# Kernel optimization log

Measured on AMD Instinct MI355X. Metric: run time of the kernel, lower is better.

The kernel has to match this reference:

```python
import jax, jax.numpy as jnp
import numpy as np

NUM_HEADS = 8
OUT_FEATS = 64
TOPK_T = 10          # settings['T']
NEG_INF = -9e15

N_NODES = 8192
IN_FEATS = 512
N_EDGES = 262144  # avg degree 32


def setup_inputs() -> dict:
    key = jax.random.key(0)
    k1, k2, k3, k4, k5 = jax.random.split(key, 5)
    feat = jax.random.normal(k1, (N_NODES, IN_FEATS), jnp.float32)
    # xavier-ish scale for the fc weight [H*D, in_feats]
    fc_weight = jax.random.normal(k2, (NUM_HEADS * OUT_FEATS, IN_FEATS), jnp.float32) * 0.05
    trans_m = jax.random.uniform(k3, (N_EDGES,), jnp.float32)
    src = jax.random.randint(k4, (N_EDGES,), 0, N_NODES, dtype=jnp.int32)
    dst = jax.random.randint(k5, (N_EDGES,), 0, N_NODES, dtype=jnp.int32)
    return {"feat": feat, "fc_weight": fc_weight, "trans_m": trans_m, "src": src, "dst": dst}


def reference(feat, fc_weight, trans_m, src, dst):
    N = feat.shape[0]
    # fc projection -> [N, H, D]
    feat_src = (feat @ fc_weight.T).reshape(N, NUM_HEADS, OUT_FEATS)
    # per-edge per-head dot-product score (SDDMM; same math as the gathered NxN matmul)
    fs, fd = feat_src[src], feat_src[dst]           # [Ne, H, D]
    e = jnp.einsum('ehd,ehd->eh', fs, fd)           # [Ne, H]
    # sparse attn values = sum over heads of e * trans_m, scattered into dense [N, N]
    vals = (e * trans_m[:, None]).sum(-1)           # [Ne]
    attn_dense = jnp.zeros((N, N), feat.dtype).at[src, dst].add(vals)
    # topk mask per row: threshold = clamp(kth largest, min=0); below -> -9e15
    thresh = jnp.maximum(jax.lax.top_k(attn_dense, TOPK_T)[0][:, -1], 0.0)  # [N]
    masked = jnp.where(attn_dense < thresh[:, None], NEG_INF, attn_dense)
    # attn = masked.T ; gather attn[src, dst] == masked[dst, src]; mask edges where < -100
    cond = masked[dst, src] < -100.0                # [Ne]
    e = jnp.where(cond[:, None], NEG_INF, e)
    # edge_softmax over incoming edges of each dst node
    emax = jax.ops.segment_max(e, dst, num_segments=N)        # [N, H]
    e_exp = jnp.exp(e - emax[dst])                            # [Ne, H]
    esum = jax.ops.segment_sum(e_exp, dst, num_segments=N)    # [N, H]
    a = e_exp / esum[dst]                                     # [Ne, H]
    # u_mul_e + sum aggregation: rst[v] = sum_{(u,v) in E} a * feat_src[u]
    rst = jax.ops.segment_sum(a[:, :, None] * fs, dst, num_segments=N)  # [N, H, D]
    return rst
```

## Files before the change

kernel.cpp:

```cpp
#include <hip/hip_runtime.h>
#include <hip/hip_bf16.h>
#include <math.h>

#define N_NODES 8192
#define IN_FEATS 512
#define N_EDGES 262144
#define NUM_HEADS 8
#define OUT_FEATS 64
#define HD (NUM_HEADS * OUT_FEATS)
#define TOPK 10
#define NEG_INF -9e15f
#define MAXD 128
#define EID_MASK 0x3FFFF

__device__ __forceinline__ int swz(int row, int k4) {
  return k4 ^ (4 * (((row & 7) ^ ((row >> 3) & 7)) & 7));
}

__global__ __launch_bounds__(512, 2) void gemm_nt(const float* __restrict__ A,
                                                  const float* __restrict__ B,
                                                  float* __restrict__ C,
                                                  ushort* __restrict__ C16) {
  __shared__ char smem[65536];
  int tid = threadIdx.x;
  int sub = tid >> 8;
  int stid = tid & 255;
  int tx = stid & 15, ty = stid >> 4;
  int brow = blockIdx.x * 128, bcol = blockIdx.y * 128;
  int kbase = sub * 256;

  float (*Asub)[32] = (float(*)[32])(smem + sub * 16384);
  float (*Bsub)[32] = (float(*)[32])(smem + 32768 + sub * 16384);

  int sr = stid >> 1;
  int skc = (stid & 1) * 8;
  const float* gA = A + (size_t)(brow + sr) * IN_FEATS + kbase + skc;
  const float* gB = B + (size_t)(bcol + sr) * IN_FEATS + kbase + skc;
  int w0 = swz(sr, skc), w1 = swz(sr, skc + 4);

  float acc[8][8];
#pragma unroll
  for (int i = 0; i < 8; i++)
#pragma unroll
    for (int j = 0; j < 8; j++) acc[i][j] = 0.f;

  float4 ra0 = *(const float4*)gA;
  float4 ra1 = *(const float4*)(gA + 4);
  float4 rb0 = *(const float4*)gB;
  float4 rb1 = *(const float4*)(gB + 4);

  const int NT = 16;
  for (int t = 0; t < NT; ++t) {
    __syncthreads();
    *(float4*)&Asub[sr][w0] = ra0; *(float4*)&Asub[sr][w1] = ra1;
    *(float4*)&Bsub[sr][w0] = rb0; *(float4*)&Bsub[sr][w1] = rb1;
    if (t + 1 < NT) {
      const float* pA = gA + (t + 1) * 16;
      const float* pB = gB + (t + 1) * 16;
      ra0 = *(const float4*)pA; ra1 = *(const float4*)(pA + 4);
      rb0 = *(const float4*)pB; rb1 = *(const float4*)(pB + 4);
    }
    __syncthreads();
#pragma unroll
    for (int g = 0; g < 4; ++g) {
      float4 av[8], bv[8];
#pragma unroll
      for (int i = 0; i < 8; i++) {
        int r = ty * 8 + i;
        av[i] = *(const float4*)&Asub[r][swz(r, g * 4)];
      }
#pragma unroll
      for (int j = 0; j < 8; j++) {
        int c = tx * 8 + j;
        bv[j] = *(const float4*)&Bsub[c][swz(c, g * 4)];
      }
#pragma unroll
      for (int i = 0; i < 8; i++)
#pragma unroll
        for (int j = 0; j < 8; j++) {
          acc[i][j] = fmaf(av[i].x, bv[j].x, acc[i][j]);
          acc[i][j] = fmaf(av[i].y, bv[j].y, acc[i][j]);
          acc[i][j] = fmaf(av[i].z, bv[j].z, acc[i][j]);
          acc[i][j] = fmaf(av[i].w, bv[j].w, acc[i][j]);
        }
    }
  }

  float (*xch)[33] = (float(*)[33])smem;
  __syncthreads();
#pragma unroll
  for (int r = 0; r < 2; ++r) {
    if (sub == 1) {
#pragma unroll
      for (int k = 0; k < 32; ++k) {
        int idx = r * 32 + k;
        xch[stid][k] = acc[idx >> 3][idx & 7];
      }
    }
    __syncthreads();
    if (sub == 0) {
#pragma unroll
      for (int k = 0; k < 32; ++k) {
        int idx = r * 32 + k;
        acc[idx >> 3][idx & 7] += xch[stid][k];
      }
    }
    __syncthreads();
  }

  if (sub == 0) {
#pragma unroll
    for (int i = 0; i < 8; i++) {
      int row = brow + ty * 8 + i;
      float* cp = C + (size_t)row * HD + bcol + tx * 8;
      *(float4*)cp = make_float4(acc[i][0], acc[i][1], acc[i][2], acc[i][3]);
      *(float4*)(cp + 4) = make_float4(acc[i][4], acc[i][5], acc[i][6], acc[i][7]);
      ushort u[8];
#pragma unroll
      for (int j = 0; j < 8; j++) u[j] = __bfloat16_as_ushort(__float2bfloat16(acc[i][j]));
      uint4 q;
      q.x = (unsigned)u[0] | ((unsigned)u[1] << 16);
      q.y = (unsigned)u[2] | ((unsigned)u[3] << 16);
      q.z = (unsigned)u[4] | ((unsigned)u[5] << 16);
      q.w = (unsigned)u[6] | ((unsigned)u[7] << 16);
      *(uint4*)(C16 + (size_t)row * HD + bcol + tx * 8) = q;
    }
  }
}

__global__ __launch_bounds__(256) void histo(const int* __restrict__ src, const int* __restrict__ dst,
                                             int* __restrict__ cnt_s, int* __restrict__ cnt_d) {
  int e = blockIdx.x * blockDim.x + threadIdx.x;
  if (e < N_EDGES) {
    atomicAdd(&cnt_s[src[e]], 1);
    atomicAdd(&cnt_d[dst[e]], 1);
  }
}

__global__ __launch_bounds__(1024) void scan2(const int* __restrict__ cnt_s, const int* __restrict__ cnt_d,
                                              int* __restrict__ rp_s, int* __restrict__ rp_d) {
  __shared__ int ls[1024];
  const int* cnt = blockIdx.x ? cnt_d : cnt_s;
  int* rp = blockIdx.x ? rp_d : rp_s;
  int t = threadIdx.x;
  int base = t * 8;
  int v[8]; int s = 0;
#pragma unroll
  for (int i = 0; i < 8; i++) { v[i] = cnt[base + i]; s += v[i]; }
  ls[t] = s;
  __syncthreads();
  for (int off = 1; off < 1024; off <<= 1) {
    int x = (t >= off) ? ls[t - off] : 0;
    __syncthreads();
    ls[t] += x;
    __syncthreads();
  }
  int excl = (t == 0) ? 0 : ls[t - 1];
#pragma unroll
  for (int i = 0; i < 8; i++) { rp[base + i] = excl; excl += v[i]; }
  if (t == 1023) rp[N_NODES] = excl;
}

__global__ __launch_bounds__(256) void scatter_csr(const int* __restrict__ src, const int* __restrict__ dst,
                                                   const int* __restrict__ rp_s, const int* __restrict__ rp_d,
                                                   int* __restrict__ fill_s, int* __restrict__ fill_d,
                                                   int* __restrict__ cs, int* __restrict__ cd) {
  int e = blockIdx.x * blockDim.x + threadIdx.x;
  if (e < N_EDGES) {
    int p = rp_s[src[e]] + atomicAdd(&fill_s[src[e]], 1);
    cs[p] = e;
    int q = rp_d[dst[e]] + atomicAdd(&fill_d[dst[e]], 1);
    cd[q] = e;
  }
}

__global__ __launch_bounds__(256) void sort_rows_bitonic(const int* __restrict__ rp_s,
                                                         const int* __restrict__ rp_d,
                                                         const int* __restrict__ dst,
                                                         int* __restrict__ cs, int* __restrict__ cd,
                                                         int* __restrict__ keys_s) {
  int wave = (blockIdx.x * blockDim.x + threadIdx.x) >> 6;
  int lane = threadIdx.x & 63;
  bool is_s = wave < N_NODES;
  int r = is_s ? wave : wave - N_NODES;
  const int* rp = is_s ? rp_s : rp_d;
  int b = rp[r], e2 = rp[r + 1];
  int len = e2 - b; if (len > 128) len = 128;

  int x0 = 0x7FFFFFFF, x1 = 0x7FFFFFFF;
  if (lane < len) {
    int e = is_s ? cs[b + lane] : cd[b + lane];
    x0 = is_s ? ((dst[e] << 18) | e) : e;
  }
  if (lane + 64 < len) {
    int e = is_s ? cs[b + lane + 64] : cd[b + lane + 64];
    x1 = is_s ? ((dst[e] << 18) | e) : e;
  }

  for (int s = 2; s <= 64; s <<= 1) {
    bool asc1 = ((64 & s) == 0);
    for (int d = s >> 1; d >= 1; d >>= 1) {
      {
        int y = __shfl_xor(x0, d);
        bool keepmin = (((lane & d) == 0) == ((lane & s) == 0));
        x0 = keepmin ? min(x0, y) : max(x0, y);
      }
      {
        int y = __shfl_xor(x1, d);
        bool asc = asc1 ? ((lane & s) == 0) : false;
        bool keepmin = (((lane & d) == 0) == asc);
        x1 = keepmin ? min(x1, y) : max(x1, y);
      }
    }
  }
  { int lo = min(x0, x1), hi = max(x0, x1); x0 = lo; x1 = hi; }
  for (int d = 32; d >= 1; d >>= 1) {
    {
      int y = __shfl_xor(x0, d);
      bool keepmin = ((lane & d) == 0);
      x0 = keepmin ? min(x0, y) : max(x0, y);
    }
    {
      int y = __shfl_xor(x1, d);
      bool keepmin = ((lane & d) == 0);
      x1 = keepmin ? min(x1, y) : max(x1, y);
    }
  }

  if (lane < len) {
    if (is_s) { cs[b + lane] = x0 & EID_MASK; keys_s[b + lane] = x0; }
    else cd[b + lane] = x0;
  }
  if (lane + 64 < len) {
    if (is_s) { cs[b + lane + 64] = x1 & EID_MASK; keys_s[b + lane + 64] = x1; }
    else cd[b + lane + 64] = x1;
  }
}

__global__ __launch_bounds__(256) void edge_scores_row(const float* __restrict__ fsrc,
                                                       const int* __restrict__ dst,
                                                       const float* __restrict__ trans,
                                                       const int* __restrict__ rp_s,
                                                       const int* __restrict__ cs,
                                                       float* __restrict__ escore, float* __restrict__ val) {
  int wave = (blockIdx.x * blockDim.x + threadIdx.x) >> 6;
  int lane = threadIdx.x & 63;
  if (wave >= N_NODES) return;
  int b = rp_s[wave], e2 = rp_s[wave + 1];
  if (b == e2) return;
  const float4* ps = (const float4*)(fsrc + (size_t)wave * HD) + lane * 2;
  float4 s0 = ps[0], s1 = ps[1];
  int head = lane >> 3;
  bool leader = (lane & 7) == 0;
  for (int i = b; i < e2; i += 4) {
    int n = e2 - i; if (n > 4) n = 4;
    int ee[4];
    float4 d0[4], d1[4];
#pragma unroll
    for (int k = 0; k < 4; k++) {
      int idx = (k < n) ? (i + k) : i;
      int e = cs[idx];
      ee[k] = e;
      const float4* pd = (const float4*)(fsrc + (size_t)dst[e] * HD) + lane * 2;
      d0[k] = pd[0];
      d1[k] = pd[1];
    }
#pragma unroll
    for (int k = 0; k < 4; k++) {
      if (k < n) {
        float dot = s0.x * d0[k].x + s0.y * d0[k].y + s0.z * d0[k].z + s0.w * d0[k].w
                  + s1.x * d1[k].x + s1.y * d1[k].y + s1.z * d1[k].z + s1.w * d1[k].w;
        dot += __shfl_xor(dot, 1);
        dot += __shfl_xor(dot, 2);
        dot += __shfl_xor(dot, 4);
        int e = ee[k];
        if (leader) escore[(size_t)e * 8 + head] = dot;
        float x = leader ? dot * trans[e] : 0.f;
        x += __shfl_xor(x, 8);
        x += __shfl_xor(x, 16);
        x += __shfl_xor(x, 32);
        if (lane == 0) val[e] = x;
      }
    }
  }
}

__global__ __launch_bounds__(256) void topk_wave(const int* __restrict__ rp_s,
                                                 const int* __restrict__ keys_s,
                                                 const float* __restrict__ val,
                                                 float* __restrict__ aval,
                                                 float* __restrict__ thresh) {
  int wave = (blockIdx.x * blockDim.x + threadIdx.x) >> 6;
  int lane = threadIdx.x & 63;
  if (wave >= N_NODES) return;
  int b = rp_s[wave], e2 = rp_s[wave + 1];
  int len = e2 - b; if (len > 128) len = 128;
  float c[2];
#pragma unroll
  for (int k = 0; k < 2; k++) {
    int i = lane + 64 * k;
    float cv = 0.f;
    if (i < len) {
      int key = keys_s[b + i];
      int d = key >> 18;
      int prevd = (i == 0) ? -1 : (keys_s[b + i - 1] >> 18);
      if (d != prevd) {
        float s = val[key & EID_MASK];
        for (int j = i + 1; j < len; j++) {
          int kj = keys_s[b + j];
          if ((kj >> 18) != d) break;
          s += val[kj & EID_MASK];
        }
        cv = s;
        aval[b + i] = s;
      } else {
        aval[b + i] = 0.f;
      }
    }
    c[k] = cv;
  }
  float t10 = 0.f;
  for (int t = 0; t < 10; t++) {
    float m = fmaxf(c[0], c[1]);
#pragma unroll
    for (int off = 1; off < 64; off <<= 1) m = fmaxf(m, __shfl_xor(m, off));
    if (m <= 0.f) { t10 = 0.f; break; }
    t10 = m;
    if (t == 9) break;
    unsigned long long b0 = __ballot(c[0] == m);
    if (b0) {
      int l = __ffsll(b0) - 1;
      if (lane == l) c[0] = -1e30f;
    } else {
      unsigned long long b1 = __ballot(c[1] == m);
      int l = __ffsll(b1) - 1;
      if (lane == l) c[1] = -1e30f;
    }
  }
  if (lane == 0) thresh[wave] = fmaxf(t10, 0.f);
}

__global__ __launch_bounds__(256) void cond_edges(const int* __restrict__ src, const int* __restrict__ dst,
                                                  const int* __restrict__ rp_s,
                                                  const int* __restrict__ keys_s,
                                                  const float* __restrict__ aval,
                                                  const float* __restrict__ thresh,
                                                  unsigned char* __restrict__ cond) {
  int e = blockIdx.x * blockDim.x + threadIdx.x;
  if (e >= N_EDGES) return;
  int s = src[e], d = dst[e];
  int lo = rp_s[d], hi = rp_s[d + 1];
  int end = hi;
  int target = s << 18;
  while (lo < hi) {
    int mid = (lo + hi) >> 1;
    if (keys_s[mid] < target) lo = mid + 1; else hi = mid;
  }
  float a = 0.f;
  if (lo < end && (keys_s[lo] >> 18) == s) a = aval[lo];
  cond[e] = (a < thresh[d]) ? 1 : 0;
}

__global__ __launch_bounds__(64) void dst_softmax_agg(const int* __restrict__ rp_d, const int* __restrict__ cd,
                                                      const int* __restrict__ src,
                                                      const unsigned char* __restrict__ cond,
                                                      const float* __restrict__ escore,
                                                      const ushort* __restrict__ fsrc16,
                                                      float* __restrict__ out) {
  __shared__ float p_lds[MAXD * 9];
  __shared__ int u_lds[MAXD];
  int v = blockIdx.x;
  int lane = threadIdx.x;
  int rb = rp_d[v], re = rp_d[v + 1];
  int d = re - rb;
  if (d > MAXD) d = MAXD;

  float sc[2][8];
  float m[8];
#pragma unroll
  for (int h = 0; h < 8; h++) m[h] = -3.0e38f;

#pragma unroll
  for (int k = 0; k < 2; k++) {
    int il = lane + 64 * k;
    if (il < d) {
      int ei = cd[rb + il];
      int u = src[ei];
      u_lds[il] = u;
      bool cmask = cond[ei] != 0;
      const float* sp = escore + (size_t)ei * 8;
      float4 s0 = *(const float4*)sp;
      float4 s1 = *(const float4*)(sp + 4);
      float ss[8] = {s0.x, s0.y, s0.z, s0.w, s1.x, s1.y, s1.z, s1.w};
#pragma unroll
      for (int h = 0; h < 8; h++) {
        float x = cmask ? NEG_INF : ss[h];
        sc[k][h] = x;
        m[h] = fmaxf(m[h], x);
      }
    } else {
#pragma unroll
      for (int h = 0; h < 8; h++) sc[k][h] = -3.0e38f;
    }
  }
#pragma unroll
  for (int off = 1; off < 64; off <<= 1)
#pragma unroll
    for (int h = 0; h < 8; h++) m[h] = fmaxf(m[h], __shfl_xor(m[h], off));

  float z[8];
#pragma unroll
  for (int h = 0; h < 8; h++) z[h] = 0.f;
#pragma unroll
  for (int k = 0; k < 2; k++) {
    int il = lane + 64 * k;
    if (il < d) {
#pragma unroll
      for (int h = 0; h < 8; h++) {
        float p = expf(sc[k][h] - m[h]);
        z[h] += p;
        p_lds[il * 9 + h] = p;
      }
    }
  }
#pragma unroll
  for (int off = 1; off < 64; off <<= 1)
#pragma unroll
    for (int h = 0; h < 8; h++) z[h] += __shfl_xor(z[h], off);

  int myh = lane >> 3;
  float zh = 0.f;
#pragma unroll
  for (int h = 0; h < 8; h++) zh = (h == myh) ? z[h] : zh;
  float invZ = (d > 0) ? (1.0f / zh) : 0.f;

  __syncthreads();

  float accA[8], accB[8];
#pragma unroll
  for (int j = 0; j < 8; j++) { accA[j] = 0.f; accB[j] = 0.f; }
  int i = 0;
  for (; i + 2 <= d; i += 2) {
    float wA = p_lds[i * 9 + myh] * invZ;
    float wB = p_lds[(i + 1) * 9 + myh] * invZ;
    const ushort* fpA = fsrc16 + (size_t)u_lds[i] * HD + lane * 8;
    const ushort* fpB = fsrc16 + (size_t)u_lds[i + 1] * HD + lane * 8;
    uint4 qA = *(const uint4*)fpA;
    uint4 qB = *(const uint4*)fpB;
    accA[0] = fmaf(wA, __uint_as_float(qA.x << 16), accA[0]);
    accA[1] = fmaf(wA, __uint_as_float(qA.x & 0xFFFF0000u), accA[1]);
    accA[2] = fmaf(wA, __uint_as_float(qA.y << 16), accA[2]);
    accA[3] = fmaf(wA, __uint_as_float(qA.y & 0xFFFF0000u), accA[3]);
    accA[4] = fmaf(wA, __uint_as_float(qA.z << 16), accA[4]);
    accA[5] = fmaf(wA, __uint_as_float(qA.z & 0xFFFF0000u), accA[5]);
    accA[6] = fmaf(wA, __uint_as_float(qA.w << 16), accA[6]);
    accA[7] = fmaf(wA, __uint_as_float(qA.w & 0xFFFF0000u), accA[7]);
    accB[0] = fmaf(wB, __uint_as_float(qB.x << 16), accB[0]);
    accB[1] = fmaf(wB, __uint_as_float(qB.x & 0xFFFF0000u), accB[1]);
    accB[2] = fmaf(wB, __uint_as_float(qB.y << 16), accB[2]);
    accB[3] = fmaf(wB, __uint_as_float(qB.y & 0xFFFF0000u), accB[3]);
    accB[4] = fmaf(wB, __uint_as_float(qB.z << 16), accB[4]);
    accB[5] = fmaf(wB, __uint_as_float(qB.z & 0xFFFF0000u), accB[5]);
    accB[6] = fmaf(wB, __uint_as_float(qB.w << 16), accB[6]);
    accB[7] = fmaf(wB, __uint_as_float(qB.w & 0xFFFF0000u), accB[7]);
  }
  if (i < d) {
    float w = p_lds[i * 9 + myh] * invZ;
    const ushort* fp = fsrc16 + (size_t)u_lds[i] * HD + lane * 8;
    uint4 q = *(const uint4*)fp;
    accA[0] = fmaf(w, __uint_as_float(q.x << 16), accA[0]);
    accA[1] = fmaf(w, __uint_as_float(q.x & 0xFFFF0000u), accA[1]);
    accA[2] = fmaf(w, __uint_as_float(q.y << 16), accA[2]);
    accA[3] = fmaf(w, __uint_as_float(q.y & 0xFFFF0000u), accA[3]);
    accA[4] = fmaf(w, __uint_as_float(q.z << 16), accA[4]);
    accA[5] = fmaf(w, __uint_as_float(q.z & 0xFFFF0000u), accA[5]);
    accA[6] = fmaf(w, __uint_as_float(q.w << 16), accA[6]);
    accA[7] = fmaf(w, __uint_as_float(q.w & 0xFFFF0000u), accA[7]);
  }
  float* op = out + (size_t)v * HD + lane * 8;
  *(float4*)op = make_float4(accA[0] + accB[0], accA[1] + accB[1], accA[2] + accB[2], accA[3] + accB[3]);
  *(float4*)(op + 4) = make_float4(accA[4] + accB[4], accA[5] + accB[5], accA[6] + accB[6], accA[7] + accB[7]);
}

extern "C" void kernel_launch(void* const* d_in, const int* in_sizes, int n_in,
                              void* d_out, int out_size, void* d_ws, size_t ws_size,
                              hipStream_t stream) {
  const float* feat = (const float*)d_in[0];
  const float* fcw = (const float*)d_in[1];
  const float* trans = (const float*)d_in[2];
  const int* src = (const int*)d_in[3];
  const int* dst = (const int*)d_in[4];
  float* out = (float*)d_out;

  char* ws = (char*)d_ws;
  size_t off = 0;
  auto alloc = [&](size_t bytes) -> void* {
    size_t o = off;
    off = (off + bytes + 255) & ~(size_t)255;
    return (void*)(ws + o);
  };
  float* fsrc = (float*)alloc((size_t)N_NODES * HD * 4);
  ushort* fsrc16 = (ushort*)alloc((size_t)N_NODES * HD * 2);
  float* escore = (float*)alloc((size_t)N_EDGES * 8 * 4);
  float* val = (float*)alloc((size_t)N_EDGES * 4);
  int* cnt = (int*)alloc((size_t)4 * N_NODES * 4);
  int* rp_s = (int*)alloc((size_t)(N_NODES + 1) * 4);
  int* rp_d = (int*)alloc((size_t)(N_NODES + 1) * 4);
  int* cs = (int*)alloc((size_t)N_EDGES * 4);
  int* cd = (int*)alloc((size_t)N_EDGES * 4);
  int* keys_s = (int*)alloc((size_t)N_EDGES * 4);
  float* aval = (float*)alloc((size_t)N_EDGES * 4);
  float* thresh = (float*)alloc((size_t)N_NODES * 4);
  unsigned char* cond = (unsigned char*)alloc((size_t)N_EDGES);
  if (off > ws_size) return;

  int* cnt_s = cnt;
  int* cnt_d = cnt + N_NODES;
  int* fill_s = cnt + 2 * N_NODES;
  int* fill_d = cnt + 3 * N_NODES;

  hipMemsetAsync(cnt, 0, (size_t)4 * N_NODES * 4, stream);
  histo<<<N_EDGES / 256, 256, 0, stream>>>(src, dst, cnt_s, cnt_d);
  scan2<<<2, 1024, 0, stream>>>(cnt_s, cnt_d, rp_s, rp_d);
  scatter_csr<<<N_EDGES / 256, 256, 0, stream>>>(src, dst, rp_s, rp_d, fill_s, fill_d, cs, cd);
  sort_rows_bitonic<<<(2 * N_NODES * 64) / 256, 256, 0, stream>>>(rp_s, rp_d, dst, cs, cd, keys_s);
  gemm_nt<<<dim3(N_NODES / 128, HD / 128), 512, 0, stream>>>(feat, fcw, fsrc, fsrc16);
  edge_scores_row<<<(N_NODES * 64) / 256, 256, 0, stream>>>(fsrc, dst, trans, rp_s, cs, escore, val);
  topk_wave<<<(N_NODES * 64) / 256, 256, 0, stream>>>(rp_s, keys_s, val, aval, thresh);
  cond_edges<<<N_EDGES / 256, 256, 0, stream>>>(src, dst, rp_s, keys_s, aval, thresh, cond);
  dst_softmax_agg<<<N_NODES, 64, 0, stream>>>(rp_d, cd, src, cond, escore, fsrc16, out);
}
```

Before: 253.4 us.

## Bucket edges by destination range for cache-local scoring; split GEMM K four ways

```diff
diff --git a/kernel.cpp b/kernel.cpp
--- a/kernel.cpp
+++ b/kernel.cpp
@@ -12,31 +12,34 @@
 #define NEG_INF -9e15f
 #define MAXD 128
 #define EID_MASK 0x3FFFF
+#define NGRP 8
+#define GRP_SHIFT 10
 
 __device__ __forceinline__ int swz(int row, int k4) {
   return k4 ^ (4 * (((row & 7) ^ ((row >> 3) & 7)) & 7));
 }
 
-__global__ __launch_bounds__(512, 2) void gemm_nt(const float* __restrict__ A,
-                                                  const float* __restrict__ B,
-                                                  float* __restrict__ C,
-                                                  ushort* __restrict__ C16) {
+__global__ __launch_bounds__(1024, 4) void gemm_nt(const float* __restrict__ A,
+                                                   const float* __restrict__ B,
+                                                   float* __restrict__ C,
+                                                   ushort* __restrict__ C16) {
   __shared__ char smem[65536];
   int tid = threadIdx.x;
   int sub = tid >> 8;
   int stid = tid & 255;
   int tx = stid & 15, ty = stid >> 4;
   int brow = blockIdx.x * 128, bcol = blockIdx.y * 128;
-  int kbase = sub * 256;
-
-  float (*Asub)[32] = (float(*)[32])(smem + sub * 16384);
-  float (*Bsub)[32] = (float(*)[32])(smem + 32768 + sub * 16384);
+  int kbase = sub * 128;
+
+  float (*Asub)[16] = (float(*)[16])(smem + sub * 8192);
+  float (*Bsub)[16] = (float(*)[16])(smem + 32768 + sub * 8192);
 
   int sr = stid >> 1;
   int skc = (stid & 1) * 8;
   const float* gA = A + (size_t)(brow + sr) * IN_FEATS + kbase + skc;
   const float* gB = B + (size_t)(bcol + sr) * IN_FEATS + kbase + skc;
-  int w0 = swz(sr, skc), w1 = swz(sr, skc + 4);
+  int w0 = (skc ^ (4 * ((sr ^ (sr >> 3)) & 1))) & 15;
+  int w1 = w0 ^ 4;
 
   float acc[8][8];
 #pragma unroll
@@ -49,7 +52,7 @@
   float4 rb0 = *(const float4*)gB;
   float4 rb1 = *(const float4*)(gB + 4);
 
-  const int NT = 16;
+  const int NT = 8;
   for (int t = 0; t < NT; ++t) {
     __syncthreads();
     *(float4*)&Asub[sr][w0] = ra0; *(float4*)&Asub[sr][w1] = ra1;
@@ -67,12 +70,14 @@
 #pragma unroll
       for (int i = 0; i < 8; i++) {
         int r = ty * 8 + i;
-        av[i] = *(const float4*)&Asub[r][swz(r, g * 4)];
+        int c = (g * 4) ^ (4 * ((r ^ (r >> 3)) & 1));
+        av[i] = *(const float4*)&Asub[r][c & 15];
       }
 #pragma unroll
       for (int j = 0; j < 8; j++) {
-        int c = tx * 8 + j;
-        bv[j] = *(const float4*)&Bsub[c][swz(c, g * 4)];
+        int c2 = tx * 8 + j;
+        int c = (g * 4) ^ (4 * ((c2 ^ (c2 >> 3)) & 1));
+        bv[j] = *(const float4*)&Bsub[c2][c & 15];
       }
 #pragma unroll
       for (int i = 0; i < 8; i++)
@@ -90,22 +95,25 @@
   __syncthreads();
 #pragma unroll
   for (int r = 0; r < 2; ++r) {
-    if (sub == 1) {
-#pragma unroll
-      for (int k = 0; k < 32; ++k) {
-        int idx = r * 32 + k;
-        xch[stid][k] = acc[idx >> 3][idx & 7];
-      }
-    }
-    __syncthreads();
-    if (sub == 0) {
-#pragma unroll
-      for (int k = 0; k < 32; ++k) {
-        int idx = r * 32 + k;
-        acc[idx >> 3][idx & 7] += xch[stid][k];
-      }
-    }
-    __syncthreads();
+#pragma unroll
+    for (int q = 1; q < 4; ++q) {
+      if (sub == q) {
+#pragma unroll
+        for (int k = 0; k < 32; ++k) {
+          int idx = r * 32 + k;
+          xch[stid][k] = acc[idx >> 3][idx & 7];
+        }
+      }
+      __syncthreads();
+      if (sub == 0) {
+#pragma unroll
+        for (int k = 0; k < 32; ++k) {
+          int idx = r * 32 + k;
+          acc[idx >> 3][idx & 7] += xch[stid][k];
+        }
+      }
+      __syncthreads();
+    }
   }
 
   if (sub == 0) {
@@ -178,7 +186,8 @@
                                                          const int* __restrict__ rp_d,
                                                          const int* __restrict__ dst,
                                                          int* __restrict__ cs, int* __restrict__ cd,
-                                                         int* __restrict__ keys_s) {
+                                                         int* __restrict__ keys_s,
+                                                         int* __restrict__ grp_off) {
   int wave = (blockIdx.x * blockDim.x + threadIdx.x) >> 6;
   int lane = threadIdx.x & 63;
   bool is_s = wave < N_NODES;
@@ -235,52 +244,58 @@
     if (is_s) { cs[b + lane + 64] = x1 & EID_MASK; keys_s[b + lane + 64] = x1; }
     else cd[b + lane + 64] = x1;
   }
-}
-
-__global__ __launch_bounds__(256) void edge_scores_row(const float* __restrict__ fsrc,
-                                                       const int* __restrict__ dst,
-                                                       const float* __restrict__ trans,
-                                                       const int* __restrict__ rp_s,
-                                                       const int* __restrict__ cs,
-                                                       float* __restrict__ escore, float* __restrict__ val) {
-  int wave = (blockIdx.x * blockDim.x + threadIdx.x) >> 6;
+
+  if (is_s) {
+    if (lane == 0) grp_off[r * NGRP] = b;
+    if (lane >= 1 && lane < NGRP) {
+      int bound = lane << (GRP_SHIFT + 18);
+      int cnt = __popcll(__ballot(x0 < bound)) + __popcll(__ballot(x1 < bound));
+      grp_off[r * NGRP + lane] = b + cnt;
+    } else {
+      __ballot(x0 < 0); __ballot(x1 < 0);
+    }
+  }
+}
+
+__global__ __launch_bounds__(256) void edge_scores_tiled(const float* __restrict__ fsrc,
+                                                         const int* __restrict__ dst,
+                                                         const float* __restrict__ trans,
+                                                         const int* __restrict__ rp_s,
+                                                         const int* __restrict__ cs,
+                                                         const int* __restrict__ grp_off,
+                                                         float* __restrict__ escore, float* __restrict__ val) {
+  int g = blockIdx.x & 7;
+  int sb = blockIdx.x >> 3;
+  int w = threadIdx.x >> 6;
   int lane = threadIdx.x & 63;
-  if (wave >= N_NODES) return;
-  int b = rp_s[wave], e2 = rp_s[wave + 1];
-  if (b == e2) return;
-  const float4* ps = (const float4*)(fsrc + (size_t)wave * HD) + lane * 2;
-  float4 s0 = ps[0], s1 = ps[1];
   int head = lane >> 3;
   bool leader = (lane & 7) == 0;
-  for (int i = b; i < e2; i += 4) {
-    int n = e2 - i; if (n > 4) n = 4;
-    int ee[4];
-    float4 d0[4], d1[4];
-#pragma unroll
-    for (int k = 0; k < 4; k++) {
-      int idx = (k < n) ? (i + k) : i;
-      int e = cs[idx];
-      ee[k] = e;
+  int rbase = sb * 32 + w * 8;
+#pragma unroll 1
+  for (int rr = 0; rr < 8; ++rr) {
+    int r = rbase + rr;
+    int b = grp_off[r * NGRP + g];
+    int e2 = (g == 7) ? rp_s[r + 1] : grp_off[r * NGRP + g + 1];
+    int cap = rp_s[r] + 128;
+    if (e2 > cap) e2 = cap;
+    if (b >= e2) continue;
+    const float4* ps = (const float4*)(fsrc + (size_t)r * HD) + lane * 2;
+    float4 s0 = ps[0], s1 = ps[1];
+    for (int i = b; i < e2; i++) {
+      int e = cs[i];
       const float4* pd = (const float4*)(fsrc + (size_t)dst[e] * HD) + lane * 2;
-      d0[k] = pd[0];
-      d1[k] = pd[1];
-    }
-#pragma unroll
-    for (int k = 0; k < 4; k++) {
-      if (k < n) {
-        float dot = s0.x * d0[k].x + s0.y * d0[k].y + s0.z * d0[k].z + s0.w * d0[k].w
-                  + s1.x * d1[k].x + s1.y * d1[k].y + s1.z * d1[k].z + s1.w * d1[k].w;
-        dot += __shfl_xor(dot, 1);
-        dot += __shfl_xor(dot, 2);
-        dot += __shfl_xor(dot, 4);
-        int e = ee[k];
-        if (leader) escore[(size_t)e * 8 + head] = dot;
-        float x = leader ? dot * trans[e] : 0.f;
-        x += __shfl_xor(x, 8);
-        x += __shfl_xor(x, 16);
-        x += __shfl_xor(x, 32);
-        if (lane == 0) val[e] = x;
-      }
+      float4 d0 = pd[0], d1 = pd[1];
+      float dot = s0.x * d0.x + s0.y * d0.y + s0.z * d0.z + s0.w * d0.w
+                + s1.x * d1.x + s1.y * d1.y + s1.z * d1.z + s1.w * d1.w;
+      dot += __shfl_xor(dot, 1);
+      dot += __shfl_xor(dot, 2);
+      dot += __shfl_xor(dot, 4);
+      if (leader) escore[(size_t)e * 8 + head] = dot;
+      float x = leader ? dot * trans[e] : 0.f;
+      x += __shfl_xor(x, 8);
+      x += __shfl_xor(x, 16);
+      x += __shfl_xor(x, 32);
+      if (lane == 0) val[e] = x;
     }
   }
 }
@@ -511,6 +526,7 @@
   int* keys_s = (int*)alloc((size_t)N_EDGES * 4);
   float* aval = (float*)alloc((size_t)N_EDGES * 4);
   float* thresh = (float*)alloc((size_t)N_NODES * 4);
+  int* grp_off = (int*)alloc((size_t)N_NODES * NGRP * 4);
   unsigned char* cond = (unsigned char*)alloc((size_t)N_EDGES);
   if (off > ws_size) return;
 
@@ -523,9 +539,9 @@
   histo<<<N_EDGES / 256, 256, 0, stream>>>(src, dst, cnt_s, cnt_d);
   scan2<<<2, 1024, 0, stream>>>(cnt_s, cnt_d, rp_s, rp_d);
   scatter_csr<<<N_EDGES / 256, 256, 0, stream>>>(src, dst, rp_s, rp_d, fill_s, fill_d, cs, cd);
-  sort_rows_bitonic<<<(2 * N_NODES * 64) / 256, 256, 0, stream>>>(rp_s, rp_d, dst, cs, cd, keys_s);
-  gemm_nt<<<dim3(N_NODES / 128, HD / 128), 512, 0, stream>>>(feat, fcw, fsrc, fsrc16);
-  edge_scores_row<<<(N_NODES * 64) / 256, 256, 0, stream>>>(fsrc, dst, trans, rp_s, cs, escore, val);
+  sort_rows_bitonic<<<(2 * N_NODES * 64) / 256, 256, 0, stream>>>(rp_s, rp_d, dst, cs, cd, keys_s, grp_off);
+  gemm_nt<<<dim3(N_NODES / 128, HD / 128), 1024, 0, stream>>>(feat, fcw, fsrc, fsrc16);
+  edge_scores_tiled<<<NGRP * (N_NODES / 32), 256, 0, stream>>>(fsrc, dst, trans, rp_s, cs, grp_off, escore, val);
   topk_wave<<<(N_NODES * 64) / 256, 256, 0, stream>>>(rp_s, keys_s, val, aval, thresh);
   cond_edges<<<N_EDGES / 256, 256, 0, stream>>>(src, dst, rp_s, keys_s, aval, thresh, cond);
   dst_softmax_agg<<<N_NODES, 64, 0, stream>>>(rp_d, cd, src, cond, escore, fsrc16, out);
```

Measured after the change: 679.5 us. +168.1%, slower.
